# Optimization experiments

Measured on AMD Instinct MI355X. Metric: run time of the kernel, lower is better.

## Reference

```python
import jax, jax.numpy as jnp
import numpy as np

EPS = 1e-6
CHI2_THRESH = 9.0
DIST_SCALE = 3.0


def _normalize(x, axis=1, eps=EPS):
    n = jnp.linalg.norm(x, axis=axis, keepdims=True)
    return x / jnp.maximum(n, eps)


def _skew(k):
    # k: (B,3) -> (B,3,3)
    kx, ky, kz = k[:, 0], k[:, 1], k[:, 2]
    O = jnp.zeros_like(kx)
    row0 = jnp.stack([O, -kz, ky], axis=1)
    row1 = jnp.stack([kz, O, -kx], axis=1)
    row2 = jnp.stack([-ky, kx, O], axis=1)
    return jnp.stack([row0, row1, row2], axis=1)


def gravity_align(g_src, g_tgt, eps=EPS):
    # Rodrigues rotation aligning g_src to g_tgt, batch-safe.
    u = _normalize(g_src, eps=eps)
    v = _normalize(g_tgt, eps=eps)
    axis = jnp.cross(u, v)
    axis_norm = jnp.linalg.norm(axis, axis=1, keepdims=True)
    dot = jnp.clip(jnp.sum(u * v, axis=1, keepdims=True), -1.0, 1.0)
    parallel = axis_norm < 1e-6
    k = axis / (axis_norm + eps)
    theta = jnp.arccos(dot)
    sin_t, cos_t = jnp.sin(theta), jnp.cos(theta)
    K = _skew(k)
    I = jnp.eye(3, dtype=g_src.dtype)[None]
    R = I + sin_t[:, :, None] * K + (1.0 - cos_t)[:, :, None] * (K @ K)
    # anti-parallel branch (computed unconditionally, selected via where)
    ex = jnp.array([1.0, 0.0, 0.0], dtype=u.dtype)[None]
    ey = jnp.array([0.0, 1.0, 0.0], dtype=u.dtype)[None]
    use_ex = jnp.abs(u[:, 0:1]) < 0.9
    basis = jnp.where(use_ex, ex, ey)
    axis2 = _normalize(jnp.cross(u, basis), eps=eps)
    K2 = _skew(axis2)
    R_anti = I + 2.0 * (K2 @ K2)
    antipar = parallel & (dot < 0.0)
    R = jnp.where(antipar[:, :, None], R_anti, R)
    R = jnp.where((parallel & (dot > 0.0))[:, :, None], I, R)
    return R


def _lower_median(x, axis):
    # torch.median(dim): lower median for even length
    n = x.shape[axis]
    return jnp.sort(x, axis=axis).take(indices=(n - 1) // 2, axis=axis)


def setup_inputs() -> dict:
    key = jax.random.key(0)
    ks = jax.random.split(key, 8)
    B, N = 4, 4096
    src = jax.random.normal(ks[0], (B, 3, N), jnp.float32)
    tgt = jax.random.normal(ks[1], (B, 3, N), jnp.float32)
    src_n = _normalize(jax.random.normal(ks[2], (B, 3, N), jnp.float32))
    tgt_n = _normalize(jax.random.normal(ks[3], (B, 3, N), jnp.float32))
    g_p = jax.random.normal(ks[4], (B, 3), jnp.float32)
    g_q = jax.random.normal(ks[5], (B, 3), jnp.float32)
    k_p = jax.random.uniform(ks[6], (B, 1), jnp.float32) + 0.1
    k_q = jax.random.uniform(ks[7], (B, 1), jnp.float32) + 0.1
    return {"src": src, "tgt": tgt, "src_n": src_n, "tgt_n": tgt_n,
            "g_p": g_p, "k_p": k_p, "g_q": g_q, "k_q": k_q}


def reference(src, tgt, src_n, tgt_n, g_p, k_p, g_q, k_q):
    B, _, N = src.shape
    R_g = gravity_align(g_p, g_q)  # (B,3,3)
    src_rot = jnp.einsum('bij,bjn->bin', R_g, src)
    src_n_rot = jnp.einsum('bij,bjn->bin', R_g, src_n)
    t_center = tgt.mean(axis=2, keepdims=True) - src_rot.mean(axis=2, keepdims=True)
    src_init = src_rot + t_center  # (B,3,N)

    # squared pairwise distances: (B,N,N)
    inner = -2.0 * jnp.einsum('bcn,bcm->bnm', src_init, tgt)
    xx = jnp.sum(src_init ** 2, axis=1)[:, :, None]
    yy = jnp.sum(tgt ** 2, axis=1)[:, None, :]
    dist_pq = xx + inner + yy

    min_pq = jnp.min(dist_pq, axis=2)
    corr_p2q = jnp.argmin(dist_pq, axis=2)
    min_qp = jnp.min(dist_pq, axis=1)
    corr_q2p = jnp.argmin(dist_pq, axis=1)

    nn_d_p = jnp.sqrt(jnp.maximum(min_pq, 0.0) + EPS)
    nn_d_q = jnp.sqrt(jnp.maximum(min_qp, 0.0) + EPS)
    tau_p = DIST_SCALE * _lower_median(nn_d_p, axis=1)[:, None]
    tau_q = DIST_SCALE * _lower_median(nn_d_q, axis=1)[:, None]
    geom_p = (nn_d_p <= tau_p).astype(src.dtype)
    geom_q = (nn_d_q <= tau_q).astype(src.dtype)

    tgt_n_matched_for_p = jnp.take_along_axis(tgt_n, corr_p2q[:, None, :], axis=2)
    src_n_matched_for_q = jnp.take_along_axis(src_n_rot, corr_q2p[:, None, :], axis=2)

    gq = g_q[:, :, None]
    inc_p = jnp.sum(src_n_rot * gq, axis=1)
    inc_p_ref = jnp.sum(tgt_n_matched_for_p * gq, axis=1)
    inc_q = jnp.sum(tgt_n * gq, axis=1)
    inc_q_ref = jnp.sum(src_n_matched_for_q * gq, axis=1)

    k_eff = k_p * k_q / (k_p + k_q + EPS)  # (B,1), broadcasts over N
    w_p = jax.nn.sigmoid(CHI2_THRESH - k_eff * (inc_p - inc_p_ref) ** 2) * geom_p
    w_q = jax.nn.sigmoid(CHI2_THRESH - k_eff * (inc_q - inc_q_ref) ** 2) * geom_q
    return w_p[:, None, :], w_q[:, None, :]
```

## Files before the change

kernel.cpp:

```cpp
#include <hip/hip_runtime.h>
#include <math.h>

#define NPTS 4096
#define NB 4
#define EPSF 1e-6f

__device__ __forceinline__ void gravity_align_rt(
    const float* __restrict__ g_p, const float* __restrict__ g_q,
    const float* sums, int b, float* R_out, float* t_out) {
    float gpx = g_p[3 * b + 0], gpy = g_p[3 * b + 1], gpz = g_p[3 * b + 2];
    float gqx = g_q[3 * b + 0], gqy = g_q[3 * b + 1], gqz = g_q[3 * b + 2];
    float nu = sqrtf(gpx * gpx + gpy * gpy + gpz * gpz);
    float du = fmaxf(nu, EPSF);
    float ux = gpx / du, uy = gpy / du, uz = gpz / du;
    float nv = sqrtf(gqx * gqx + gqy * gqy + gqz * gqz);
    float dv = fmaxf(nv, EPSF);
    float vx = gqx / dv, vy = gqy / dv, vz = gqz / dv;

    float ax = uy * vz - uz * vy;
    float ay = uz * vx - ux * vz;
    float az = ux * vy - uy * vx;
    float an = sqrtf(ax * ax + ay * ay + az * az);
    float dot = ux * vx + uy * vy + uz * vz;
    dot = fminf(1.0f, fmaxf(-1.0f, dot));
    bool parallel = (an < 1e-6f);

    float kx = ax / (an + EPSF), ky = ay / (an + EPSF), kz = az / (an + EPSF);
    float theta = acosf(dot);
    float st = sinf(theta), ct = cosf(theta);

    float K[9] = {0.f, -kz, ky,  kz, 0.f, -kx,  -ky, kx, 0.f};
    float KK[9];
    for (int i = 0; i < 3; ++i)
        for (int j = 0; j < 3; ++j) {
            float s2 = 0.f;
            for (int l = 0; l < 3; ++l) s2 += K[i * 3 + l] * K[l * 3 + j];
            KK[i * 3 + j] = s2;
        }
    float R[9];
    for (int i = 0; i < 9; ++i) {
        float I = (i == 0 || i == 4 || i == 8) ? 1.f : 0.f;
        R[i] = I + st * K[i] + (1.f - ct) * KK[i];
    }
    if (parallel) {
        if (dot < 0.f) {
            float bx, by, bz;
            if (fabsf(ux) < 0.9f) { bx = 1.f; by = 0.f; bz = 0.f; }
            else                  { bx = 0.f; by = 1.f; bz = 0.f; }
            float cx = uy * bz - uz * by;
            float cy = uz * bx - ux * bz;
            float cz = ux * by - uy * bx;
            float cn = sqrtf(cx * cx + cy * cy + cz * cz);
            float cd = fmaxf(cn, EPSF);
            cx /= cd; cy /= cd; cz /= cd;
            float K2[9] = {0.f, -cz, cy,  cz, 0.f, -cx,  -cy, cx, 0.f};
            float K2K2[9];
            for (int i = 0; i < 3; ++i)
                for (int j = 0; j < 3; ++j) {
                    float s2 = 0.f;
                    for (int l = 0; l < 3; ++l) s2 += K2[i * 3 + l] * K2[l * 3 + j];
                    K2K2[i * 3 + j] = s2;
                }
            for (int i = 0; i < 9; ++i) {
                float I = (i == 0 || i == 4 || i == 8) ? 1.f : 0.f;
                R[i] = I + 2.f * K2K2[i];
            }
        } else if (dot > 0.f) {
            for (int i = 0; i < 9; ++i) R[i] = (i == 0 || i == 4 || i == 8) ? 1.f : 0.f;
        }
    }
    float ms0 = sums[0] / (float)NPTS, ms1 = sums[1] / (float)NPTS, ms2 = sums[2] / (float)NPTS;
    float mt0 = sums[3] / (float)NPTS, mt1 = sums[4] / (float)NPTS, mt2 = sums[5] / (float)NPTS;
    for (int i = 0; i < 9; ++i) R_out[i] = R[i];
    t_out[0] = mt0 - (R[0] * ms0 + R[1] * ms1 + R[2] * ms2);
    t_out[1] = mt1 - (R[3] * ms0 + R[4] * ms1 + R[5] * ms2);
    t_out[2] = mt2 - (R[6] * ms0 + R[7] * ms1 + R[8] * ms2);
}

__global__ void k0_setup(const float* __restrict__ src, const float* __restrict__ tgt,
                         const float* __restrict__ src_n, const float* __restrict__ tgt_n,
                         const float* __restrict__ g_p, const float* __restrict__ g_q,
                         float4* __restrict__ p4, float4* __restrict__ q4,
                         float4* __restrict__ snr4, float4* __restrict__ tn4) {
    const int b = blockIdx.x;
    const int tid = threadIdx.x;
    const float* S  = src   + (size_t)b * 3 * NPTS;
    const float* T  = tgt   + (size_t)b * 3 * NPTS;
    const float* SN = src_n + (size_t)b * 3 * NPTS;
    const float* TN = tgt_n + (size_t)b * 3 * NPTS;

    __shared__ float red[256];
    __shared__ float sums[6];
    __shared__ float Rg[9], tc[3];

    float acc[6] = {0.f, 0.f, 0.f, 0.f, 0.f, 0.f};
    if (tid < 256) {
        for (int n = tid; n < NPTS; n += 256) {
            acc[0] += S[n]; acc[1] += S[NPTS + n]; acc[2] += S[2 * NPTS + n];
            acc[3] += T[n]; acc[4] += T[NPTS + n]; acc[5] += T[2 * NPTS + n];
        }
    }
    for (int c = 0; c < 6; ++c) {
        if (tid < 256) red[tid] = acc[c];
        __syncthreads();
        for (int s = 128; s > 0; s >>= 1) {
            if (tid < s) red[tid] += red[tid + s];
            __syncthreads();
        }
        if (tid == 0) sums[c] = red[0];
        __syncthreads();
    }

    if (tid == 0) gravity_align_rt(g_p, g_q, sums, b, Rg, tc);
    __syncthreads();

    const float R0 = Rg[0], R1 = Rg[1], R2 = Rg[2];
    const float R3 = Rg[3], R4 = Rg[4], R5 = Rg[5];
    const float R6 = Rg[6], R7 = Rg[7], R8 = Rg[8];
    const float t0 = tc[0], t1 = tc[1], t2 = tc[2];

    for (int n = tid; n < NPTS; n += 1024) {
        float s0 = S[n], s1 = S[NPTS + n], s2 = S[2 * NPTS + n];
        float p0 = R0 * s0 + R1 * s1 + R2 * s2 + t0;
        float p1 = R3 * s0 + R4 * s1 + R5 * s2 + t1;
        float p2 = R6 * s0 + R7 * s1 + R8 * s2 + t2;
        p4[b * NPTS + n] = make_float4(p0, p1, p2, p0 * p0 + p1 * p1 + p2 * p2);

        float q0 = T[n], q1 = T[NPTS + n], q2 = T[2 * NPTS + n];
        q4[b * NPTS + n] = make_float4(q0, q1, q2, q0 * q0 + q1 * q1 + q2 * q2);

        float a0 = SN[n], a1 = SN[NPTS + n], a2 = SN[2 * NPTS + n];
        snr4[b * NPTS + n] = make_float4(R0 * a0 + R1 * a1 + R2 * a2,
                                         R3 * a0 + R4 * a1 + R5 * a2,
                                         R6 * a0 + R7 * a1 + R8 * a2, 0.f);
        float c0 = TN[n], c1 = TN[NPTS + n], c2 = TN[2 * NPTS + n];
        tn4[b * NPTS + n] = make_float4(c0, c1, c2, 0.f);
    }
}

__global__ void k1_nn(const float4* __restrict__ p4, const float4* __restrict__ q4,
                      float* __restrict__ nnp, int* __restrict__ idxp,
                      float* __restrict__ nnq, int* __restrict__ idxq) {
    const int b = blockIdx.y;
    const int z = blockIdx.z;
    const float4* own = z ? q4 : p4;
    const float4* oth = z ? p4 : q4;
    float* nn = z ? nnq : nnp;
    int* idx = z ? idxq : idxp;

    __shared__ float4 stage[NPTS];
    const int tid = threadIdx.x;
    for (int i = tid; i < NPTS; i += 1024) {
        float4 v = oth[b * NPTS + i];
        v.w *= -0.5f;
        stage[i] = v;
    }

    const int nl = tid & 63;
    const int stripe = tid >> 6;
    const int n = blockIdx.x * 64 + nl;
    const float4 p = own[b * NPTS + n];
    __syncthreads();

    const int m0 = stripe << 8;
    float best = -3.4e38f;
    int bi = m0;
    #pragma unroll 8
    for (int m = m0; m < m0 + 256; ++m) {
        float4 q = stage[m];
        float s = fmaf(p.x, q.x, fmaf(p.y, q.y, fmaf(p.z, q.z, q.w)));
        if (s > best) { best = s; bi = m; }
    }
    __syncthreads();

    float* combd = (float*)stage;
    int* combi = (int*)(combd + 1024);
    combd[tid] = best;
    combi[tid] = bi;
    __syncthreads();
    if (stripe == 0) {
        for (int s2 = 1; s2 < 16; ++s2) {
            float d2 = combd[s2 * 64 + nl];
            int i2 = combi[s2 * 64 + nl];
            if (d2 > best) { best = d2; bi = i2; }
        }
        float d = fmaf(-2.0f, best, p.w);
        nn[b * NPTS + n] = sqrtf(fmaxf(d, 0.f) + EPSF);
        idx[b * NPTS + n] = bi;
    }
}

__global__ void kc_tau_w(const float* __restrict__ nnp, const float* __restrict__ nnq,
                         const float4* __restrict__ snr4, const float4* __restrict__ tn4,
                         const int* __restrict__ idxp, const int* __restrict__ idxq,
                         const float* __restrict__ g_q, const float* __restrict__ k_p,
                         const float* __restrict__ k_q, float* __restrict__ out) {
    const int b = blockIdx.x;
    const int z = blockIdx.y;
    const int tid = threadIdx.x;
    const int wid = tid >> 6;
    const int lane = tid & 63;
    const float* a = (z ? nnq : nnp) + b * NPTS;

    unsigned int v[4];
    float vf[4];
    #pragma unroll
    for (int j = 0; j < 4; ++j) {
        float x = a[tid + j * 1024];
        vf[j] = x;
        v[j] = __float_as_uint(x);
    }

    __shared__ int hist[16][256];
    __shared__ int tot[256];
    __shared__ int digit_s, base_s;

    const int shifts[4]   = {23, 15, 7, 0};
    const unsigned him[4] = {0x00000000u, 0x7F800000u, 0x7FFF8000u, 0x7FFFFF80u};
    const unsigned dm[4]  = {0xFFu, 0xFFu, 0xFFu, 0x7Fu};

    unsigned int prefix = 0u;
    int rank = 2047;

    for (int p = 0; p < 4; ++p) {
        const int sh = shifts[p];
        const unsigned himask = him[p];
        const unsigned dmask = dm[p];

        for (int k2 = lane; k2 < 256; k2 += 64) hist[wid][k2] = 0;
        __syncthreads();

        #pragma unroll
        for (int j = 0; j < 4; ++j) {
            if ((v[j] & himask) == prefix)
                atomicAdd(&hist[wid][(v[j] >> sh) & dmask], 1);
        }
        __syncthreads();

        if (tid < 256) {
            int t = 0;
            #pragma unroll
            for (int w = 0; w < 16; ++w) t += hist[w][tid];
            tot[tid] = t;
        }
        __syncthreads();

        if (wid == 0) {
            int c0 = tot[4 * lane + 0], c1 = tot[4 * lane + 1];
            int c2 = tot[4 * lane + 2], c3 = tot[4 * lane + 3];
            int s = c0 + c1 + c2 + c3;
            int incl = s;
            #pragma unroll
            for (int o = 1; o < 64; o <<= 1) {
                int t = __shfl_up(incl, o, 64);
                if (lane >= o) incl += t;
            }
            int base = incl - s;
            int cs[4] = {c0, c1, c2, c3};
            #pragma unroll
            for (int k2 = 0; k2 < 4; ++k2) {
                if (cs[k2] > 0 && rank >= base && rank < base + cs[k2]) {
                    digit_s = 4 * lane + k2;
                    base_s = base;
                }
                base += cs[k2];
            }
        }
        __syncthreads();
        prefix |= ((unsigned)digit_s) << sh;
        rank -= base_s;
        __syncthreads();
    }
    const float tauv = 3.0f * __uint_as_float(prefix);

    const float gx = g_q[3 * b + 0], gy = g_q[3 * b + 1], gz = g_q[3 * b + 2];
    const float kp = k_p[b], kq = k_q[b];
    const float keff = kp * kq / (kp + kq + EPSF);

    #pragma unroll
    for (int j = 0; j < 4; ++j) {
        const int n = tid + j * 1024;
        float w;
        if (z == 0) {
            float4 sn = snr4[b * NPTS + n];
            float inc = sn.x * gx + sn.y * gy + sn.z * gz;
            int jj = idxp[b * NPTS + n];
            float4 tn = tn4[b * NPTS + jj];
            float incr = tn.x * gx + tn.y * gy + tn.z * gz;
            float diff = inc - incr;
            float arg = 9.0f - keff * diff * diff;
            float sig = 1.f / (1.f + expf(-arg));
            float geom = (vf[j] <= tauv) ? 1.f : 0.f;
            w = sig * geom;
        } else {
            float4 tn = tn4[b * NPTS + n];
            float inc = tn.x * gx + tn.y * gy + tn.z * gz;
            int jj = idxq[b * NPTS + n];
            float4 sn = snr4[b * NPTS + jj];
            float incr = sn.x * gx + sn.y * gy + sn.z * gz;
            float diff = inc - incr;
            float arg = 9.0f - keff * diff * diff;
            float sig = 1.f / (1.f + expf(-arg));
            float geom = (vf[j] <= tauv) ? 1.f : 0.f;
            w = sig * geom;
        }
        out[z * (NB * NPTS) + b * NPTS + n] = w;
    }
}

extern "C" void kernel_launch(void* const* d_in, const int* in_sizes, int n_in,
                              void* d_out, int out_size, void* d_ws, size_t ws_size,
                              hipStream_t stream) {
    const float* src   = (const float*)d_in[0];
    const float* tgt   = (const float*)d_in[1];
    const float* src_n = (const float*)d_in[2];
    const float* tgt_n = (const float*)d_in[3];
    const float* g_p   = (const float*)d_in[4];
    const float* k_p   = (const float*)d_in[5];
    const float* g_q   = (const float*)d_in[6];
    const float* k_q   = (const float*)d_in[7];
    float* out = (float*)d_out;

    const int BN = NB * NPTS;
    float4* p4   = (float4*)d_ws;
    float4* q4   = p4 + BN;
    float4* snr4 = q4 + BN;
    float4* tn4  = snr4 + BN;
    float* nnp = (float*)(tn4 + BN);
    float* nnq = nnp + BN;
    int* idxp = (int*)(nnq + BN);
    int* idxq = idxp + BN;

    k0_setup<<<dim3(NB), dim3(1024), 0, stream>>>(src, tgt, src_n, tgt_n, g_p, g_q,
                                                  p4, q4, snr4, tn4);
    k1_nn<<<dim3(NPTS / 64, NB, 2), dim3(1024), 0, stream>>>(p4, q4, nnp, idxp, nnq, idxq);
    kc_tau_w<<<dim3(NB, 2), dim3(1024), 0, stream>>>(nnp, nnq, snr4, tn4, idxp, idxq,
                                                     g_q, k_p, k_q, out);
}
```

Measured before the change: 53.28 us.

## Fuse setup, nearest-neighbor, and median/weight stages into one persistent kernel with grid barrier

Result: slower. 88.34 us (+65.8%).

```diff
diff --git a/kernel.cpp b/kernel.cpp
--- a/kernel.cpp
+++ b/kernel.cpp
@@ -75,6 +75,257 @@
     t_out[0] = mt0 - (R[0] * ms0 + R[1] * ms1 + R[2] * ms2);
     t_out[1] = mt1 - (R[3] * ms0 + R[4] * ms1 + R[5] * ms2);
     t_out[2] = mt2 - (R[6] * ms0 + R[7] * ms1 + R[8] * ms2);
+}
+
+__global__ __launch_bounds__(1024, 8) void mega2(
+    const float* __restrict__ src, const float* __restrict__ tgt,
+    const float* __restrict__ src_n, const float* __restrict__ tgt_n,
+    const float* __restrict__ g_p, const float* __restrict__ g_q,
+    const float* __restrict__ k_p, const float* __restrict__ k_q,
+    float* __restrict__ nnp, int* __restrict__ idxp,
+    float* __restrict__ nnq, int* __restrict__ idxq,
+    unsigned int* __restrict__ bar, float* __restrict__ out)
+{
+    const int tid = threadIdx.x;
+    const int bid = blockIdx.x;
+    const int x = bid & 63;
+    const int b = (bid >> 6) & 3;
+    const int z = bid >> 8;
+
+    __shared__ float4 stage4[NPTS];
+    float* sf = (float*)stage4;
+    int* si = (int*)stage4;
+
+    const float* S  = src   + (size_t)b * 3 * NPTS;
+    const float* T  = tgt   + (size_t)b * 3 * NPTS;
+    const float* SN = src_n + (size_t)b * 3 * NPTS;
+    const float* TN = tgt_n + (size_t)b * 3 * NPTS;
+
+    {
+        float acc[6] = {0.f, 0.f, 0.f, 0.f, 0.f, 0.f};
+        if (tid < 256) {
+            for (int n = tid; n < NPTS; n += 256) {
+                acc[0] += S[n]; acc[1] += S[NPTS + n]; acc[2] += S[2 * NPTS + n];
+                acc[3] += T[n]; acc[4] += T[NPTS + n]; acc[5] += T[2 * NPTS + n];
+            }
+        }
+        if (tid < 256) {
+            #pragma unroll
+            for (int c = 0; c < 6; ++c) sf[c * 256 + tid] = acc[c];
+        }
+        __syncthreads();
+        for (int s = 128; s > 0; s >>= 1) {
+            if (tid < s) {
+                #pragma unroll
+                for (int c = 0; c < 6; ++c) sf[c * 256 + tid] += sf[c * 256 + tid + s];
+            }
+            __syncthreads();
+        }
+        if (tid == 0) {
+            float sums[6];
+            #pragma unroll
+            for (int c = 0; c < 6; ++c) sums[c] = sf[c * 256];
+            gravity_align_rt(g_p, g_q, sums, b, sf + 1536, sf + 1545);
+        }
+        __syncthreads();
+    }
+    const float R0 = sf[1536], R1 = sf[1537], R2 = sf[1538];
+    const float R3 = sf[1539], R4 = sf[1540], R5 = sf[1541];
+    const float R6 = sf[1542], R7 = sf[1543], R8 = sf[1544];
+    const float t0 = sf[1545], t1 = sf[1546], t2 = sf[1547];
+    __syncthreads();
+
+    const int nl = tid & 63;
+    const int stripe = tid >> 6;
+    const int n = x * 64 + nl;
+    float4 p;
+    {
+        if (z == 0) {
+            for (int i = tid; i < NPTS; i += 1024) {
+                float q0 = T[i], q1 = T[NPTS + i], q2 = T[2 * NPTS + i];
+                float w = (q0 * q0 + q1 * q1 + q2 * q2) * -0.5f;
+                stage4[i] = make_float4(q0, q1, q2, w);
+            }
+            float s0 = S[n], s1 = S[NPTS + n], s2 = S[2 * NPTS + n];
+            float p0 = R0 * s0 + R1 * s1 + R2 * s2 + t0;
+            float p1 = R3 * s0 + R4 * s1 + R5 * s2 + t1;
+            float p2 = R6 * s0 + R7 * s1 + R8 * s2 + t2;
+            p = make_float4(p0, p1, p2, p0 * p0 + p1 * p1 + p2 * p2);
+        } else {
+            for (int i = tid; i < NPTS; i += 1024) {
+                float s0 = S[i], s1 = S[NPTS + i], s2 = S[2 * NPTS + i];
+                float p0 = R0 * s0 + R1 * s1 + R2 * s2 + t0;
+                float p1 = R3 * s0 + R4 * s1 + R5 * s2 + t1;
+                float p2 = R6 * s0 + R7 * s1 + R8 * s2 + t2;
+                float w = (p0 * p0 + p1 * p1 + p2 * p2) * -0.5f;
+                stage4[i] = make_float4(p0, p1, p2, w);
+            }
+            float q0 = T[n], q1 = T[NPTS + n], q2 = T[2 * NPTS + n];
+            p = make_float4(q0, q1, q2, q0 * q0 + q1 * q1 + q2 * q2);
+        }
+        __syncthreads();
+
+        const int m0 = stripe << 8;
+        float best = -3.4e38f;
+        int bi = m0;
+        #pragma unroll 8
+        for (int m = m0; m < m0 + 256; ++m) {
+            float4 q = stage4[m];
+            float s = fmaf(p.x, q.x, fmaf(p.y, q.y, fmaf(p.z, q.z, q.w)));
+            if (s > best) { best = s; bi = m; }
+        }
+        __syncthreads();
+
+        float* combd = sf;
+        int* combi = (int*)(combd + 1024);
+        combd[tid] = best;
+        combi[tid] = bi;
+        __syncthreads();
+        if (stripe == 0) {
+            for (int s2 = 1; s2 < 16; ++s2) {
+                float d2 = combd[s2 * 64 + nl];
+                int i2 = combi[s2 * 64 + nl];
+                if (d2 > best) { best = d2; bi = i2; }
+            }
+            float d = fmaf(-2.0f, best, p.w);
+            float* nn = z ? nnq : nnp;
+            int* idx = z ? idxq : idxp;
+            nn[b * NPTS + n] = sqrtf(fmaxf(d, 0.f) + EPSF);
+            idx[b * NPTS + n] = bi;
+        }
+    }
+
+    __syncthreads();
+    if (tid == 0) {
+        __threadfence();
+        unsigned int old = atomicAdd(bar, 1u);
+        unsigned int target = (old & ~511u) + 512u;
+        int guard = 0;
+        while (__hip_atomic_load(bar, __ATOMIC_ACQUIRE, __HIP_MEMORY_SCOPE_AGENT) < target) {
+            __builtin_amdgcn_s_sleep(2);
+            if (++guard > (1 << 22)) break;
+        }
+        __threadfence();
+    }
+    __syncthreads();
+
+    if (x != 0) return;
+
+    const float* a = (z ? nnq : nnp) + b * NPTS;
+    unsigned int v[4];
+    float vf[4];
+    #pragma unroll
+    for (int j = 0; j < 4; ++j) {
+        float xx = a[tid + j * 1024];
+        vf[j] = xx;
+        v[j] = __float_as_uint(xx);
+    }
+
+    int* hist = si;
+    int* tot = si + 4096;
+    int* digit_s = si + 4352;
+    int* base_s = si + 4353;
+
+    const int wid = tid >> 6;
+    const int lane = tid & 63;
+    const int shifts[4]   = {23, 15, 7, 0};
+    const unsigned him[4] = {0x00000000u, 0x7F800000u, 0x7FFF8000u, 0x7FFFFF80u};
+    const unsigned dm[4]  = {0xFFu, 0xFFu, 0xFFu, 0x7Fu};
+
+    unsigned int prefix = 0u;
+    int rank = 2047;
+
+    __syncthreads();
+    for (int pss = 0; pss < 4; ++pss) {
+        const int sh = shifts[pss];
+        const unsigned himask = him[pss];
+        const unsigned dmask = dm[pss];
+
+        for (int k2 = lane; k2 < 256; k2 += 64) hist[wid * 256 + k2] = 0;
+        __syncthreads();
+
+        #pragma unroll
+        for (int j = 0; j < 4; ++j) {
+            if ((v[j] & himask) == prefix)
+                atomicAdd(&hist[wid * 256 + ((v[j] >> sh) & dmask)], 1);
+        }
+        __syncthreads();
+
+        if (tid < 256) {
+            int t = 0;
+            #pragma unroll
+            for (int w = 0; w < 16; ++w) t += hist[w * 256 + tid];
+            tot[tid] = t;
+        }
+        __syncthreads();
+
+        if (wid == 0) {
+            int c0 = tot[4 * lane + 0], c1 = tot[4 * lane + 1];
+            int c2 = tot[4 * lane + 2], c3 = tot[4 * lane + 3];
+            int s = c0 + c1 + c2 + c3;
+            int incl = s;
+            #pragma unroll
+            for (int o = 1; o < 64; o <<= 1) {
+                int t = __shfl_up(incl, o, 64);
+                if (lane >= o) incl += t;
+            }
+            int base = incl - s;
+            int cs[4] = {c0, c1, c2, c3};
+            #pragma unroll
+            for (int k2 = 0; k2 < 4; ++k2) {
+                if (cs[k2] > 0 && rank >= base && rank < base + cs[k2]) {
+                    *digit_s = 4 * lane + k2;
+                    *base_s = base;
+                }
+                base += cs[k2];
+            }
+        }
+        __syncthreads();
+        prefix |= ((unsigned)(*digit_s)) << sh;
+        rank -= *base_s;
+        __syncthreads();
+    }
+    const float tauv = 3.0f * __uint_as_float(prefix);
+
+    const float gx = g_q[3 * b + 0], gy = g_q[3 * b + 1], gz = g_q[3 * b + 2];
+    const float kp = k_p[b], kq = k_q[b];
+    const float keff = kp * kq / (kp + kq + EPSF);
+
+    #pragma unroll
+    for (int j = 0; j < 4; ++j) {
+        const int nn2 = tid + j * 1024;
+        float w;
+        if (z == 0) {
+            float a0 = SN[nn2], a1 = SN[NPTS + nn2], a2 = SN[2 * NPTS + nn2];
+            float snx = R0 * a0 + R1 * a1 + R2 * a2;
+            float sny = R3 * a0 + R4 * a1 + R5 * a2;
+            float snz = R6 * a0 + R7 * a1 + R8 * a2;
+            float inc = snx * gx + sny * gy + snz * gz;
+            int jj = idxp[b * NPTS + nn2];
+            float tnx = TN[jj], tny = TN[NPTS + jj], tnz = TN[2 * NPTS + jj];
+            float incr = tnx * gx + tny * gy + tnz * gz;
+            float diff = inc - incr;
+            float arg = 9.0f - keff * diff * diff;
+            float sig = 1.f / (1.f + expf(-arg));
+            float geom = (vf[j] <= tauv) ? 1.f : 0.f;
+            w = sig * geom;
+        } else {
+            float tnx = TN[nn2], tny = TN[NPTS + nn2], tnz = TN[2 * NPTS + nn2];
+            float inc = tnx * gx + tny * gy + tnz * gz;
+            int jj = idxq[b * NPTS + nn2];
+            float a0 = SN[jj], a1 = SN[NPTS + jj], a2 = SN[2 * NPTS + jj];
+            float snx = R0 * a0 + R1 * a1 + R2 * a2;
+            float sny = R3 * a0 + R4 * a1 + R5 * a2;
+            float snz = R6 * a0 + R7 * a1 + R8 * a2;
+            float incr = snx * gx + sny * gy + snz * gz;
+            float diff = inc - incr;
+            float arg = 9.0f - keff * diff * diff;
+            float sig = 1.f / (1.f + expf(-arg));
+            float geom = (vf[j] <= tauv) ? 1.f : 0.f;
+            w = sig * geom;
+        }
+        out[z * (NB * NPTS) + b * NPTS + nn2] = w;
+    }
 }
 
 __global__ void k0_setup(const float* __restrict__ src, const float* __restrict__ tgt,
@@ -330,10 +581,18 @@
     float* nnq = nnp + BN;
     int* idxp = (int*)(nnq + BN);
     int* idxq = idxp + BN;
-
-    k0_setup<<<dim3(NB), dim3(1024), 0, stream>>>(src, tgt, src_n, tgt_n, g_p, g_q,
-                                                  p4, q4, snr4, tn4);
-    k1_nn<<<dim3(NPTS / 64, NB, 2), dim3(1024), 0, stream>>>(p4, q4, nnp, idxp, nnq, idxq);
-    kc_tau_w<<<dim3(NB, 2), dim3(1024), 0, stream>>>(nnp, nnq, snr4, tn4, idxp, idxq,
-                                                     g_q, k_p, k_q, out);
+    unsigned int* bar = (unsigned int*)(idxq + BN);
+
+    hipError_t err = hipMemsetAsync(bar, 0, 64, stream);
+    if (err == hipSuccess) {
+        mega2<<<dim3(512), dim3(1024), 0, stream>>>(
+            src, tgt, src_n, tgt_n, g_p, g_q, k_p, k_q,
+            nnp, idxp, nnq, idxq, bar, out);
+    } else {
+        k0_setup<<<dim3(NB), dim3(1024), 0, stream>>>(src, tgt, src_n, tgt_n, g_p, g_q,
+                                                      p4, q4, snr4, tn4);
+        k1_nn<<<dim3(NPTS / 64, NB, 2), dim3(1024), 0, stream>>>(p4, q4, nnp, idxp, nnq, idxq);
+        kc_tau_w<<<dim3(NB, 2), dim3(1024), 0, stream>>>(nnp, nnq, snr4, tn4, idxp, idxq,
+                                                         g_q, k_p, k_q, out);
+    }
 }
```

## Drop intermediate float4 buffers and parallelize weight stage across point tiles

Applied to the files above, without the earlier changes.

Measured after the change: 46.55 us. -12.6%, faster.

```diff
diff --git a/kernel.cpp b/kernel.cpp
--- a/kernel.cpp
+++ b/kernel.cpp
@@ -77,31 +77,23 @@
     t_out[2] = mt2 - (R[6] * ms0 + R[7] * ms1 + R[8] * ms2);
 }
 
-__global__ void k0_setup(const float* __restrict__ src, const float* __restrict__ tgt,
-                         const float* __restrict__ src_n, const float* __restrict__ tgt_n,
-                         const float* __restrict__ g_p, const float* __restrict__ g_q,
-                         float4* __restrict__ p4, float4* __restrict__ q4,
-                         float4* __restrict__ snr4, float4* __restrict__ tn4) {
+__global__ void k0a_rt(const float* __restrict__ src, const float* __restrict__ tgt,
+                       const float* __restrict__ g_p, const float* __restrict__ g_q,
+                       float* __restrict__ Rt) {
     const int b = blockIdx.x;
     const int tid = threadIdx.x;
-    const float* S  = src   + (size_t)b * 3 * NPTS;
-    const float* T  = tgt   + (size_t)b * 3 * NPTS;
-    const float* SN = src_n + (size_t)b * 3 * NPTS;
-    const float* TN = tgt_n + (size_t)b * 3 * NPTS;
-
+    const float* S = src + (size_t)b * 3 * NPTS;
+    const float* T = tgt + (size_t)b * 3 * NPTS;
+
+    float acc[6] = {0.f, 0.f, 0.f, 0.f, 0.f, 0.f};
+    for (int n = tid; n < NPTS; n += 256) {
+        acc[0] += S[n]; acc[1] += S[NPTS + n]; acc[2] += S[2 * NPTS + n];
+        acc[3] += T[n]; acc[4] += T[NPTS + n]; acc[5] += T[2 * NPTS + n];
+    }
     __shared__ float red[256];
     __shared__ float sums[6];
-    __shared__ float Rg[9], tc[3];
-
-    float acc[6] = {0.f, 0.f, 0.f, 0.f, 0.f, 0.f};
-    if (tid < 256) {
-        for (int n = tid; n < NPTS; n += 256) {
-            acc[0] += S[n]; acc[1] += S[NPTS + n]; acc[2] += S[2 * NPTS + n];
-            acc[3] += T[n]; acc[4] += T[NPTS + n]; acc[5] += T[2 * NPTS + n];
-        }
-    }
     for (int c = 0; c < 6; ++c) {
-        if (tid < 256) red[tid] = acc[c];
+        red[tid] = acc[c];
         __syncthreads();
         for (int s = 128; s > 0; s >>= 1) {
             if (tid < s) red[tid] += red[tid + s];
@@ -110,56 +102,59 @@
         if (tid == 0) sums[c] = red[0];
         __syncthreads();
     }
-
-    if (tid == 0) gravity_align_rt(g_p, g_q, sums, b, Rg, tc);
-    __syncthreads();
-
-    const float R0 = Rg[0], R1 = Rg[1], R2 = Rg[2];
-    const float R3 = Rg[3], R4 = Rg[4], R5 = Rg[5];
-    const float R6 = Rg[6], R7 = Rg[7], R8 = Rg[8];
-    const float t0 = tc[0], t1 = tc[1], t2 = tc[2];
-
-    for (int n = tid; n < NPTS; n += 1024) {
+    if (tid == 0) {
+        float Rg[9], tc[3];
+        gravity_align_rt(g_p, g_q, sums, b, Rg, tc);
+        for (int i = 0; i < 9; ++i) Rt[b * 16 + i] = Rg[i];
+        Rt[b * 16 + 9]  = tc[0];
+        Rt[b * 16 + 10] = tc[1];
+        Rt[b * 16 + 11] = tc[2];
+    }
+}
+
+__global__ void k1r(const float* __restrict__ src, const float* __restrict__ tgt,
+                    const float* __restrict__ Rt,
+                    float* __restrict__ nnp, int* __restrict__ idxp,
+                    float* __restrict__ nnq, int* __restrict__ idxq) {
+    const int b = blockIdx.y;
+    const int z = blockIdx.z;
+    const int tid = threadIdx.x;
+    const float* S = src + (size_t)b * 3 * NPTS;
+    const float* T = tgt + (size_t)b * 3 * NPTS;
+    const float R0 = Rt[b*16+0], R1 = Rt[b*16+1], R2 = Rt[b*16+2];
+    const float R3 = Rt[b*16+3], R4 = Rt[b*16+4], R5 = Rt[b*16+5];
+    const float R6 = Rt[b*16+6], R7 = Rt[b*16+7], R8 = Rt[b*16+8];
+    const float t0 = Rt[b*16+9], t1 = Rt[b*16+10], t2 = Rt[b*16+11];
+
+    __shared__ float4 stage4[NPTS];
+    const int nl = tid & 63;
+    const int stripe = tid >> 6;
+    const int n = blockIdx.x * 64 + nl;
+    float4 p;
+
+    if (z == 0) {
+        for (int i = tid; i < NPTS; i += 1024) {
+            float q0 = T[i], q1 = T[NPTS + i], q2 = T[2 * NPTS + i];
+            float w = (q0 * q0 + q1 * q1 + q2 * q2) * -0.5f;
+            stage4[i] = make_float4(q0, q1, q2, w);
+        }
         float s0 = S[n], s1 = S[NPTS + n], s2 = S[2 * NPTS + n];
         float p0 = R0 * s0 + R1 * s1 + R2 * s2 + t0;
         float p1 = R3 * s0 + R4 * s1 + R5 * s2 + t1;
         float p2 = R6 * s0 + R7 * s1 + R8 * s2 + t2;
-        p4[b * NPTS + n] = make_float4(p0, p1, p2, p0 * p0 + p1 * p1 + p2 * p2);
-
+        p = make_float4(p0, p1, p2, p0 * p0 + p1 * p1 + p2 * p2);
+    } else {
+        for (int i = tid; i < NPTS; i += 1024) {
+            float s0 = S[i], s1 = S[NPTS + i], s2 = S[2 * NPTS + i];
+            float p0 = R0 * s0 + R1 * s1 + R2 * s2 + t0;
+            float p1 = R3 * s0 + R4 * s1 + R5 * s2 + t1;
+            float p2 = R6 * s0 + R7 * s1 + R8 * s2 + t2;
+            float w = (p0 * p0 + p1 * p1 + p2 * p2) * -0.5f;
+            stage4[i] = make_float4(p0, p1, p2, w);
+        }
         float q0 = T[n], q1 = T[NPTS + n], q2 = T[2 * NPTS + n];
-        q4[b * NPTS + n] = make_float4(q0, q1, q2, q0 * q0 + q1 * q1 + q2 * q2);
-
-        float a0 = SN[n], a1 = SN[NPTS + n], a2 = SN[2 * NPTS + n];
-        snr4[b * NPTS + n] = make_float4(R0 * a0 + R1 * a1 + R2 * a2,
-                                         R3 * a0 + R4 * a1 + R5 * a2,
-                                         R6 * a0 + R7 * a1 + R8 * a2, 0.f);
-        float c0 = TN[n], c1 = TN[NPTS + n], c2 = TN[2 * NPTS + n];
-        tn4[b * NPTS + n] = make_float4(c0, c1, c2, 0.f);
-    }
-}
-
-__global__ void k1_nn(const float4* __restrict__ p4, const float4* __restrict__ q4,
-                      float* __restrict__ nnp, int* __restrict__ idxp,
-                      float* __restrict__ nnq, int* __restrict__ idxq) {
-    const int b = blockIdx.y;
-    const int z = blockIdx.z;
-    const float4* own = z ? q4 : p4;
-    const float4* oth = z ? p4 : q4;
-    float* nn = z ? nnq : nnp;
-    int* idx = z ? idxq : idxp;
-
-    __shared__ float4 stage[NPTS];
-    const int tid = threadIdx.x;
-    for (int i = tid; i < NPTS; i += 1024) {
-        float4 v = oth[b * NPTS + i];
-        v.w *= -0.5f;
-        stage[i] = v;
-    }
-
-    const int nl = tid & 63;
-    const int stripe = tid >> 6;
-    const int n = blockIdx.x * 64 + nl;
-    const float4 p = own[b * NPTS + n];
+        p = make_float4(q0, q1, q2, q0 * q0 + q1 * q1 + q2 * q2);
+    }
     __syncthreads();
 
     const int m0 = stripe << 8;
@@ -167,13 +162,13 @@
     int bi = m0;
     #pragma unroll 8
     for (int m = m0; m < m0 + 256; ++m) {
-        float4 q = stage[m];
+        float4 q = stage4[m];
         float s = fmaf(p.x, q.x, fmaf(p.y, q.y, fmaf(p.z, q.z, q.w)));
         if (s > best) { best = s; bi = m; }
     }
     __syncthreads();
 
-    float* combd = (float*)stage;
+    float* combd = (float*)stage4;
     int* combi = (int*)(combd + 1024);
     combd[tid] = best;
     combi[tid] = bi;
@@ -185,31 +180,31 @@
             if (d2 > best) { best = d2; bi = i2; }
         }
         float d = fmaf(-2.0f, best, p.w);
+        float* nn = z ? nnq : nnp;
+        int* idx = z ? idxq : idxp;
         nn[b * NPTS + n] = sqrtf(fmaxf(d, 0.f) + EPSF);
         idx[b * NPTS + n] = bi;
     }
 }
 
-__global__ void kc_tau_w(const float* __restrict__ nnp, const float* __restrict__ nnq,
-                         const float4* __restrict__ snr4, const float4* __restrict__ tn4,
-                         const int* __restrict__ idxp, const int* __restrict__ idxq,
-                         const float* __restrict__ g_q, const float* __restrict__ k_p,
-                         const float* __restrict__ k_q, float* __restrict__ out) {
-    const int b = blockIdx.x;
-    const int z = blockIdx.y;
+__global__ void kcr(const float* __restrict__ nnp, const float* __restrict__ nnq,
+                    const int* __restrict__ idxp, const int* __restrict__ idxq,
+                    const float* __restrict__ src_n, const float* __restrict__ tgt_n,
+                    const float* __restrict__ Rt,
+                    const float* __restrict__ g_q, const float* __restrict__ k_p,
+                    const float* __restrict__ k_q, float* __restrict__ out) {
+    const int x = blockIdx.x;
+    const int b = blockIdx.y;
+    const int z = blockIdx.z;
     const int tid = threadIdx.x;
     const int wid = tid >> 6;
     const int lane = tid & 63;
     const float* a = (z ? nnq : nnp) + b * NPTS;
 
     unsigned int v[4];
-    float vf[4];
     #pragma unroll
-    for (int j = 0; j < 4; ++j) {
-        float x = a[tid + j * 1024];
-        vf[j] = x;
-        v[j] = __float_as_uint(x);
-    }
+    for (int j = 0; j < 4; ++j)
+        v[j] = __float_as_uint(a[tid + j * 1024]);
 
     __shared__ int hist[16][256];
     __shared__ int tot[256];
@@ -273,35 +268,45 @@
     }
     const float tauv = 3.0f * __uint_as_float(prefix);
 
-    const float gx = g_q[3 * b + 0], gy = g_q[3 * b + 1], gz = g_q[3 * b + 2];
-    const float kp = k_p[b], kq = k_q[b];
-    const float keff = kp * kq / (kp + kq + EPSF);
-
-    #pragma unroll
-    for (int j = 0; j < 4; ++j) {
-        const int n = tid + j * 1024;
+    if (tid < 64) {
+        const int n = x * 64 + tid;
+        const float* SN = src_n + (size_t)b * 3 * NPTS;
+        const float* TN = tgt_n + (size_t)b * 3 * NPTS;
+        const float R0 = Rt[b*16+0], R1 = Rt[b*16+1], R2 = Rt[b*16+2];
+        const float R3 = Rt[b*16+3], R4 = Rt[b*16+4], R5 = Rt[b*16+5];
+        const float R6 = Rt[b*16+6], R7 = Rt[b*16+7], R8 = Rt[b*16+8];
+        const float gx = g_q[3 * b + 0], gy = g_q[3 * b + 1], gz = g_q[3 * b + 2];
+        const float kp = k_p[b], kq = k_q[b];
+        const float keff = kp * kq / (kp + kq + EPSF);
+
         float w;
         if (z == 0) {
-            float4 sn = snr4[b * NPTS + n];
-            float inc = sn.x * gx + sn.y * gy + sn.z * gz;
+            float a0 = SN[n], a1 = SN[NPTS + n], a2 = SN[2 * NPTS + n];
+            float snx = R0 * a0 + R1 * a1 + R2 * a2;
+            float sny = R3 * a0 + R4 * a1 + R5 * a2;
+            float snz = R6 * a0 + R7 * a1 + R8 * a2;
+            float inc = snx * gx + sny * gy + snz * gz;
             int jj = idxp[b * NPTS + n];
-            float4 tn = tn4[b * NPTS + jj];
-            float incr = tn.x * gx + tn.y * gy + tn.z * gz;
+            float tnx = TN[jj], tny = TN[NPTS + jj], tnz = TN[2 * NPTS + jj];
+            float incr = tnx * gx + tny * gy + tnz * gz;
             float diff = inc - incr;
             float arg = 9.0f - keff * diff * diff;
             float sig = 1.f / (1.f + expf(-arg));
-            float geom = (vf[j] <= tauv) ? 1.f : 0.f;
+            float geom = (a[n] <= tauv) ? 1.f : 0.f;
             w = sig * geom;
         } else {
-            float4 tn = tn4[b * NPTS + n];
-            float inc = tn.x * gx + tn.y * gy + tn.z * gz;
+            float tnx = TN[n], tny = TN[NPTS + n], tnz = TN[2 * NPTS + n];
+            float inc = tnx * gx + tny * gy + tnz * gz;
             int jj = idxq[b * NPTS + n];
-            float4 sn = snr4[b * NPTS + jj];
-            float incr = sn.x * gx + sn.y * gy + sn.z * gz;
+            float a0 = SN[jj], a1 = SN[NPTS + jj], a2 = SN[2 * NPTS + jj];
+            float snx = R0 * a0 + R1 * a1 + R2 * a2;
+            float sny = R3 * a0 + R4 * a1 + R5 * a2;
+            float snz = R6 * a0 + R7 * a1 + R8 * a2;
+            float incr = snx * gx + sny * gy + snz * gz;
             float diff = inc - incr;
             float arg = 9.0f - keff * diff * diff;
             float sig = 1.f / (1.f + expf(-arg));
-            float geom = (vf[j] <= tauv) ? 1.f : 0.f;
+            float geom = (a[n] <= tauv) ? 1.f : 0.f;
             w = sig * geom;
         }
         out[z * (NB * NPTS) + b * NPTS + n] = w;
@@ -322,18 +327,16 @@
     float* out = (float*)d_out;
 
     const int BN = NB * NPTS;
-    float4* p4   = (float4*)d_ws;
-    float4* q4   = p4 + BN;
-    float4* snr4 = q4 + BN;
-    float4* tn4  = snr4 + BN;
-    float* nnp = (float*)(tn4 + BN);
+    float* nnp = (float*)d_ws;
     float* nnq = nnp + BN;
     int* idxp = (int*)(nnq + BN);
     int* idxq = idxp + BN;
-
-    k0_setup<<<dim3(NB), dim3(1024), 0, stream>>>(src, tgt, src_n, tgt_n, g_p, g_q,
-                                                  p4, q4, snr4, tn4);
-    k1_nn<<<dim3(NPTS / 64, NB, 2), dim3(1024), 0, stream>>>(p4, q4, nnp, idxp, nnq, idxq);
-    kc_tau_w<<<dim3(NB, 2), dim3(1024), 0, stream>>>(nnp, nnq, snr4, tn4, idxp, idxq,
-                                                     g_q, k_p, k_q, out);
-}
+    float* Rt  = (float*)(idxq + BN);
+
+    k0a_rt<<<dim3(NB), dim3(256), 0, stream>>>(src, tgt, g_p, g_q, Rt);
+    k1r<<<dim3(NPTS / 64, NB, 2), dim3(1024), 0, stream>>>(src, tgt, Rt,
+                                                           nnp, idxp, nnq, idxq);
+    kcr<<<dim3(NPTS / 64, NB, 2), dim3(1024), 0, stream>>>(nnp, nnq, idxp, idxq,
+                                                           src_n, tgt_n, Rt,
+                                                           g_q, k_p, k_q, out);
+}
```
